# Kernel tuning notes

Hardware: AMD Instinct MI355X
Metric: run time of the kernel (lower is better)

## Reference

```python
import jax, jax.numpy as jnp
import numpy as np

TOPK = 13
NUM_CLASSES = 80
ALPHA = 1.0
BETA = 3.0
EPS = 1e-9
K_NEAR = 4
N_BINS = 36  # theta bins: arange(0, 360, 10)


def _dist_max_per_bin(anc_points, gt_pts):
    """gt_pts: (bs,nm,360,2), anc_points: (na,2) -> (bs,nm,na,36) ray targets."""
    d = gt_pts[:, :, None, :, :] - anc_points[None, None, :, None, :]  # (bs,nm,na,360,2)
    dist = jnp.sqrt(jnp.sum(d * d, axis=-1))                           # (bs,nm,na,360)
    ang = jnp.rad2deg(jnp.arctan2(d[..., 1], d[..., 0])) % 360.0       # (bs,nm,na,360)
    theta = jnp.arange(0, 360, 360 // N_BINS).astype(ang.dtype)        # (36,)

    def per_theta(th):
        diff = jnp.abs(ang - th)
        diff = jnp.where(diff > 180.0, 360.0 - diff, diff)
        neg_v, idx = jax.lax.top_k(-diff, K_NEAR)   # 4 nearest-angle contour pts
        val = -neg_v
        dk = jnp.take_along_axis(dist, idx, axis=-1)
        dk = jnp.where(jnp.min(val, axis=-1, keepdims=True) > 3.0, 1e-6, dk)
        return jnp.max(dk, axis=-1)                 # (bs,nm,na)

    dm = jax.lax.map(per_theta, theta)              # (36,bs,nm,na); chunked to bound memory
    return jnp.maximum(jnp.moveaxis(dm, 0, -1), 1e-6)


def _mask_iou(target, pred):
    l_max = jnp.maximum(target, pred)
    l_min = jnp.maximum(jnp.minimum(target, pred), 1e-6)
    return jnp.sum(l_min, -1) / jnp.sum(l_max, -1)


def _forward(pd_scores, pd_bboxes, anc_points, gt_labels, gt_bboxes, mask_gt, gt_coor):
    bs, na, nc = pd_scores.shape
    nm = gt_bboxes.shape[1]
    gl = gt_labels[..., 0]            # (bs,nm) int
    mgt = mask_gt[..., 0]             # (bs,nm) float
    gt_pts = gt_coor.reshape(bs, nm, 360, 2)

    # select_candidates_in_gts: anchor center strictly inside gt box
    lt, rb = gt_bboxes[..., :2], gt_bboxes[..., 2:]
    deltas = jnp.concatenate([anc_points[None, None] - lt[:, :, None],
                              rb[:, :, None] - anc_points[None, None]], axis=-1)
    mask_in_gts = (jnp.min(deltas, -1) > 1e-9).astype(pd_scores.dtype)  # (bs,nm,na)
    mask_sel = (mask_in_gts * mgt[:, :, None]) > 0

    # get_box_metrics_polar (dense over (bs,nm,na) instead of boolean-mask select)
    dist_max = _dist_max_per_bin(anc_points, gt_pts)                    # (bs,nm,na,36)
    overlaps = jnp.where(mask_sel, _mask_iou(dist_max, pd_bboxes[:, None]), 0.0)
    bbox_scores = jnp.take_along_axis(jnp.swapaxes(pd_scores, 1, 2), gl[:, :, None], axis=1)
    bbox_scores = jnp.where(mask_sel, bbox_scores, 0.0)
    align_metric = (bbox_scores ** ALPHA) * (overlaps ** BETA)

    # select_topk_candidates
    _, topk_idxs = jax.lax.top_k(align_metric, TOPK)
    topk_idxs = jnp.where(mgt[:, :, None] > 0, topk_idxs, 0)
    count = jnp.sum(jax.nn.one_hot(topk_idxs, na, dtype=align_metric.dtype), axis=-2)
    mask_topk = jnp.where(count > 1, 0.0, count)
    mask_pos = mask_topk * mask_in_gts * mgt[:, :, None]

    # select_highest_overlaps
    fg = jnp.sum(mask_pos, -2)                                          # (bs,na)
    multi = fg[:, None, :] > 1
    is_max = jnp.moveaxis(jax.nn.one_hot(jnp.argmax(overlaps, 1), nm, dtype=mask_pos.dtype), -1, 1)
    mask_pos = jnp.where(multi, is_max, mask_pos)
    fg_mask = jnp.sum(mask_pos, -2)
    target_gt_idx = jnp.argmax(mask_pos, -2)                            # (bs,na)

    # per-positive ray-distance targets + polar centerness (dense, masked)
    mask_pos_b = mask_pos > 0
    gt_dist = jnp.where(mask_pos_b[..., None], dist_max, 0.0)           # (bs,nm,na,36)
    cent = jnp.sqrt(jnp.min(dist_max, -1) / jnp.max(dist_max, -1))
    centerness_gt = jnp.where(mask_pos_b, cent, 0.0)                    # (bs,nm,na)

    # get_targets
    target_labels = jnp.maximum(jnp.take_along_axis(gl, target_gt_idx, axis=1), 0)
    target_bboxes = jnp.take_along_axis(gt_bboxes, target_gt_idx[..., None], axis=1)
    target_scores = jax.nn.one_hot(target_labels, NUM_CLASSES, dtype=pd_scores.dtype)
    target_scores = jnp.where((fg_mask > 0)[..., None], target_scores, 0.0)

    am = align_metric * mask_pos
    pos_align = jnp.max(am, -1, keepdims=True)
    pos_ov = jnp.max(overlaps * mask_pos, -1, keepdims=True)
    norm_align = jnp.max(am * pos_ov / (pos_align + EPS), -2)[..., None]  # (bs,na,1)
    target_scores = target_scores * norm_align

    return (target_labels, target_bboxes, target_scores, mask_pos_b,
            target_gt_idx, gt_dist, centerness_gt, fg_mask > 0)


def setup_inputs():
    key = jax.random.key(0)
    k = jax.random.split(key, 6)
    bs, nc, nm = 2, 80, 10
    pts, strs = [], []
    for s in (8, 16, 32):  # 640x640 YOLO grid -> 8400 anchors
        n = 640 // s
        yv, xv = np.meshgrid(np.arange(n), np.arange(n), indexing='ij')
        pts.append(np.stack([(xv + 0.5) * s, (yv + 0.5) * s], -1).reshape(-1, 2))
        strs.append(np.full((pts[-1].shape[0], 1), s, dtype=np.float32))
    anc_points = jnp.asarray(np.concatenate(pts).astype(np.float32))
    stride_tensor = jnp.asarray(np.concatenate(strs))
    na = anc_points.shape[0]
    pd_scores = jax.random.uniform(k[0], (bs, na, nc), dtype=jnp.float32)
    pd_bboxes = jax.random.uniform(k[1], (bs, na, 36), dtype=jnp.float32) * 100.0 + 1.0
    gt_labels = jax.random.randint(k[2], (bs, nm, 1), 0, nc)
    ctr = jax.random.uniform(k[3], (bs, nm, 2), dtype=jnp.float32) * 440.0 + 100.0
    wh = jax.random.uniform(k[4], (bs, nm, 2), dtype=jnp.float32) * 140.0 + 40.0
    gt_bboxes = jnp.concatenate([ctr - wh / 2.0, ctr + wh / 2.0], -1)
    th = jnp.arange(360.0) * (jnp.pi / 180.0)
    rad = (jnp.min(wh, -1, keepdims=True) / 2.0) * (0.6 + 0.4 * jax.random.uniform(k[5], (bs, nm, 360), dtype=jnp.float32))
    ray = jnp.stack([jnp.cos(th), jnp.sin(th)], -1)  # (360,2)
    gt_coor = (ctr[:, :, None, :] + rad[..., None] * ray[None, None]).reshape(bs, nm, 720)
    mask_gt = jnp.ones((bs, nm, 1), dtype=jnp.float32).at[1, 7:].set(0.0)
    return dict(pd_scores=pd_scores, pd_bboxes=pd_bboxes, anc_points=anc_points,
                gt_labels=gt_labels, gt_bboxes=gt_bboxes, mask_gt=mask_gt,
                gt_coor=gt_coor, stride_tensor=stride_tensor, ss=640,
                gt_center=ctr, imgsz=640)


def reference(pd_scores, pd_bboxes, anc_points, gt_labels, gt_bboxes, mask_gt, gt_coor, stride_tensor, ss, gt_center, imgsz):
    # ss, gt_center, imgsz, stride_tensor are accepted (as in the torch signature) but unused
    return _forward(pd_scores, pd_bboxes, anc_points, gt_labels, gt_bboxes, mask_gt, gt_coor)
```

## Files before the change

kernel.cpp:

```cpp
#include <hip/hip_runtime.h>

#define BS 2
#define NM 10
#define NA 8400
#define NC 80
#define NBIN 36
#define KTOP 13
#define NRECT (BS*NM*3)
#define WDIST_CAP 16384

typedef unsigned long long ull;

__device__ __forceinline__ void rect_one(int bm, int lv,
    const float* __restrict__ gtb, const float* __restrict__ mgt,
    int& x0, int& y0, int& cx, int& cy, int& cnt, int& n, int& base){
  cnt = 0; x0 = 0; y0 = 0; cx = 0; cy = 0; n = 0; base = 0;
  if (mgt[bm] > 0.f){
    float s = (float)(8 << lv);
    n = 640 >> (3 + lv);
    base = (lv == 0) ? 0 : ((lv == 1) ? 6400 : 8000);
    float lx = gtb[bm*4+0], ly = gtb[bm*4+1];
    float rx = gtb[bm*4+2], ry = gtb[bm*4+3];
    int a0 = (int)ceilf(lx/s - 0.5f); a0 = min(max(a0, 0), n);
    while (a0 > 0   &&  (((a0-1)+0.5f)*s - lx > 1e-9f)) a0--;
    while (a0 < n   && !(((a0  )+0.5f)*s - lx > 1e-9f)) a0++;
    int a1 = (int)floorf(rx/s - 0.5f); a1 = min(max(a1, -1), n-1);
    while (a1 < n-1 &&  (rx - ((a1+1)+0.5f)*s > 1e-9f)) a1++;
    while (a1 >= 0  && !(rx - ((a1  )+0.5f)*s > 1e-9f)) a1--;
    int b0 = (int)ceilf(ly/s - 0.5f); b0 = min(max(b0, 0), n);
    while (b0 > 0   &&  (((b0-1)+0.5f)*s - ly > 1e-9f)) b0--;
    while (b0 < n   && !(((b0  )+0.5f)*s - ly > 1e-9f)) b0++;
    int b1 = (int)floorf(ry/s - 0.5f); b1 = min(max(b1, -1), n-1);
    while (b1 < n-1 &&  (ry - ((b1+1)+0.5f)*s > 1e-9f)) b1++;
    while (b1 >= 0  && !(ry - ((b1  )+0.5f)*s > 1e-9f)) b1--;
    cx = max(0, a1 - a0 + 1);
    cy = max(0, b1 - b0 + 1);
    cnt = cx * cy;
    x0 = a0; y0 = b0;
  }
}

__device__ __forceinline__ void rect_setup(int tid,
    const float* __restrict__ gtb, const float* __restrict__ mgt,
    int* sx0, int* sy0, int* scx, int* scy, int* scum, int* sn, int* sbase){
  if (tid < NRECT){
    int bm = tid/3, lv = tid - bm*3;
    int x0, y0, cx, cy, cnt, n, base;
    rect_one(bm, lv, gtb, mgt, x0, y0, cx, cy, cnt, n, base);
    sx0[tid] = x0; sy0[tid] = y0; scx[tid] = cx; scy[tid] = cy;
    scum[tid] = cnt; sn[tid] = n; sbase[tid] = base;
  }
  __syncthreads();
  if (tid == 0){
    int acc = 0;
    for (int r = 0; r < NRECT; r++){ int c = scum[r]; scum[r] = acc; acc += c; }
    scum[NRECT] = acc;
  }
  __syncthreads();
}

__device__ __forceinline__ int pair_from_p(int p,
    const int* sx0, const int* sy0, const int* scx,
    const int* scum, const int* sn, const int* sbase){
  int lo = 0, hi = NRECT - 1;
  while (lo < hi){ int mid = (lo + hi + 1) >> 1; if (scum[mid] <= p) lo = mid; else hi = mid - 1; }
  int r = lo;
  int idx = p - scum[r];
  int cx = scx[r];
  int yi = idx / cx;
  int xi = idx - yi*cx;
  int a = sbase[r] + (sy0[r] + yi)*sn[r] + (sx0[r] + xi);
  int bm = r/3;
  return bm*NA + a;
}

__device__ __forceinline__ ull shflx_u64(ull v, int off){
  unsigned lo = (unsigned)v, hi = (unsigned)(v >> 32);
  lo = __shfl_xor(lo, off); hi = __shfl_xor(hi, off);
  return ((ull)hi << 32) | lo;
}

__global__ __launch_bounds__(256)
void k_dist(const float* __restrict__ pds, const float* __restrict__ pdb,
            const float* __restrict__ anc, const int* __restrict__ gl,
            const float* __restrict__ gtb, const float* __restrict__ mgt,
            const float* __restrict__ coor,
            float* __restrict__ out, float* __restrict__ wf){
  float* o_labels  = out;
  float* o_bboxes  = o_labels + BS*NA;
  float* o_scores  = o_bboxes + BS*NA*4;
  float* o_maskpos = o_scores + (size_t)BS*NA*NC;
  float* o_gtidx   = o_maskpos + BS*NM*NA;
  float* o_gtdist  = o_gtidx + BS*NA;
  float* o_cent    = o_gtdist + (size_t)BS*NM*NA*NBIN;
  float* o_fg      = o_cent + BS*NM*NA;

  float* w_align = wf + 16;
  float* w_ovl   = w_align + BS*NM*NA;
  float* w_dist  = w_ovl + BS*NM*NA;

  __shared__ int sx0[NRECT], sy0[NRECT], scx[NRECT], scy[NRECT], scum[NRECT+1], sn[NRECT], sbase[NRECT];
  __shared__ float2 s_ad[360];
  __shared__ unsigned short s_ix[360];
  __shared__ int s_cnt[NBIN], s_off[NBIN+1], s_cur[NBIN];
  __shared__ ull  s_k[NBIN*29];
  __shared__ float s_d[NBIN*29];
  __shared__ float s_res[NBIN];
  __shared__ int s_fbl[NBIN];
  __shared__ int s_nfb;

  float2* s_tmp = (float2*)s_k;
  unsigned char* s_bu = ((unsigned char*)s_k) + 2880;

  int tid = threadIdx.x;
  int lane = tid & 63, wave = tid >> 6;

  rect_setup(tid, gtb, mgt, sx0, sy0, scx, scy, scum, sn, sbase);
  int total = scum[NRECT];

  {
    int gtid = blockIdx.x*256 + tid, gsz = gridDim.x*256;
    float4 z4 = make_float4(0.f,0.f,0.f,0.f);
    float4* zs = (float4*)o_scores;
    for (int i = gtid; i < (BS*NA*NC)/4; i += gsz) zs[i] = z4;
    float4* zg = (float4*)o_gtdist;
    for (int i = gtid; i < (BS*NM*NA*NBIN)/4; i += gsz) zg[i] = z4;
    float4* zc = (float4*)o_cent;
    for (int i = gtid; i < (BS*NM*NA)/4; i += gsz) zc[i] = z4;
    float4* zm = (float4*)o_maskpos;
    for (int i = gtid; i < (BS*NM*NA)/4; i += gsz) zm[i] = z4;
    if (gtid < 16) wf[gtid] = 0.f;
    for (int t = gtid; t < BS*NA; t += gsz){
      int b = t / NA;
      o_gtidx[t] = 0.f;
      o_fg[t] = 0.f;
      int lbl = gl[b*NM]; if (lbl < 0) lbl = 0;
      o_labels[t] = (float)lbl;
      const float* bx = gtb + (b*NM)*4;
      ((float4*)o_bboxes)[t] = make_float4(bx[0], bx[1], bx[2], bx[3]);
    }
    for (int row = gtid; row < BS*NM*NA; row += gsz){
      int bm = row / NA;
      int a  = row - bm*NA;
      int lv = (a < 6400) ? 0 : ((a < 8000) ? 1 : 2);
      int ai = a - ((lv == 0) ? 0 : ((lv == 1) ? 6400 : 8000));
      int r = bm*3 + lv;
      bool inrect = false;
      if (scx[r] > 0 && scy[r] > 0){
        int n = sn[r];
        int y = ai / n, x = ai - y*n;
        inrect = (x >= sx0[r] && x < sx0[r]+scx[r] &&
                  y >= sy0[r] && y < sy0[r]+scy[r]);
      }
      if (!inrect) w_ovl[row] = 0.f;
    }
  }

  if (tid < NBIN) s_cnt[tid] = 0;
  if (tid == 0) s_nfb = 0;
  __syncthreads();

  int bin7 = tid % 36;
  int slot7 = tid / 36;

  for (int p = blockIdx.x; p < total; p += gridDim.x){
    int t = pair_from_p(p, sx0, sy0, scx, scum, sn, sbase);
    int a = t % NA; int bm = t / NA; int b = bm / NM;
    float ax = anc[2*a], ay = anc[2*a+1];
    const float* cc = coor + bm*720;

    for (int i = tid; i < 360; i += 256){
      float dx = cc[2*i]   - ax;
      float dy = cc[2*i+1] - ay;
      float dist = sqrtf(dx*dx + dy*dy);
      float an = atan2f(dy, dx) * 57.29577951308232f;
      if (an < 0.f) an += 360.f;
      int bu = (int)(an * 0.1f); bu = min(bu, NBIN-1);
      s_tmp[i] = make_float2(an, dist);
      s_bu[i] = (unsigned char)bu;
      atomicAdd(&s_cnt[bu], 1);
    }
    __syncthreads();
    if (wave == 0){
      int c = (lane < NBIN) ? s_cnt[lane] : 0;
      int incl = c;
#pragma unroll
      for (int st = 1; st < 64; st <<= 1){
        int o = __shfl_up(incl, st);
        if (lane >= st) incl += o;
      }
      if (lane < NBIN){ s_off[lane+1] = incl; s_cur[lane] = incl - c; }
      if (lane == 0) s_off[0] = 0;
    }
    __syncthreads();
    for (int i = tid; i < 360; i += 256){
      int bu = s_bu[i];
      float2 ad = s_tmp[i];
      int pos = atomicAdd(&s_cur[bu], 1);
      s_ad[pos] = ad;
      s_ix[pos] = (unsigned short)i;
    }
    __syncthreads();

#define EVALJ(J, TH) { \
      float2 ad = s_ad[J]; \
      unsigned int ixv = s_ix[J]; \
      float df = fabsf(ad.x - (TH)); \
      df = fminf(df, 360.f - df); \
      ull key = ((ull)__float_as_uint(df) << 32) | ixv; \
      if (key < k3){ \
        k3 = key; d3 = ad.y; \
        if (k3 < k2){ ull tk=k2; k2=k3; k3=tk; float td=d2; d2=d3; d3=td; } \
        if (k2 < k1){ ull tk=k1; k1=k2; k2=tk; float td=d1; d1=d2; d2=td; } \
        if (k1 < k0){ ull tk=k0; k0=k1; k1=tk; float td=d0; d0=d1; d1=td; } \
      } }

    if (slot7 < 7){
      float th = (float)(bin7*10);
      int r0s, r0e, r1s, r1e;
      if (bin7 == 0)      { r0s = s_off[35]; r0e = s_off[36]; r1s = 0; r1e = s_off[2]; }
      else if (bin7 == 35){ r0s = s_off[34]; r0e = s_off[36]; r1s = 0; r1e = s_off[1]; }
      else                { r0s = s_off[bin7-1]; r0e = s_off[bin7+2]; r1s = 0; r1e = 0; }
      int L0 = r0e - r0s, L = L0 + (r1e - r1s);
      ull k0,k1,k2,k3; float d0,d1,d2,d3;
      k0=k1=k2=k3=~0ull; d0=d1=d2=d3=0.f;
      for (int w = slot7; w < L; w += 7){
        int j = (w < L0) ? (r0s + w) : (r1s + w - L0);
        EVALJ(j, th)
      }
      int mb = bin7*29 + slot7*4;
      s_k[mb+0]=k0; s_k[mb+1]=k1; s_k[mb+2]=k2; s_k[mb+3]=k3;
      s_d[mb+0]=d0; s_d[mb+1]=d1; s_d[mb+2]=d2; s_d[mb+3]=d3;
    }
    __syncthreads();

    if (wave == 0 && lane < NBIN){
      int mb = lane*29;
      ull h0=s_k[mb+0], h1=s_k[mb+4],  h2=s_k[mb+8],  h3=s_k[mb+12],
          h4=s_k[mb+16], h5=s_k[mb+20], h6=s_k[mb+24];
      int p0=0,p1=0,p2=0,p3=0,p4=0,p5=0,p6=0;
      float v0m = 0.f, d4v = 0.f, dmax = 0.f;
#pragma unroll
      for (int step = 0; step < 4; step++){
        ull bk = h0; int bw = 0;
        if (h1 < bk){ bk = h1; bw = 1; }
        if (h2 < bk){ bk = h2; bw = 2; }
        if (h3 < bk){ bk = h3; bw = 3; }
        if (h4 < bk){ bk = h4; bw = 4; }
        if (h5 < bk){ bk = h5; bw = 5; }
        if (h6 < bk){ bk = h6; bw = 6; }
        float dd;
        if (bw == 0){ dd = s_d[mb   +p0]; p0++; h0 = (p0<4)? s_k[mb   +p0] : ~0ull; }
        else if (bw == 1){ dd = s_d[mb+ 4+p1]; p1++; h1 = (p1<4)? s_k[mb+ 4+p1] : ~0ull; }
        else if (bw == 2){ dd = s_d[mb+ 8+p2]; p2++; h2 = (p2<4)? s_k[mb+ 8+p2] : ~0ull; }
        else if (bw == 3){ dd = s_d[mb+12+p3]; p3++; h3 = (p3<4)? s_k[mb+12+p3] : ~0ull; }
        else if (bw == 4){ dd = s_d[mb+16+p4]; p4++; h4 = (p4<4)? s_k[mb+16+p4] : ~0ull; }
        else if (bw == 5){ dd = s_d[mb+20+p5]; p5++; h5 = (p5<4)? s_k[mb+20+p5] : ~0ull; }
        else             { dd = s_d[mb+24+p6]; p6++; h6 = (p6<4)? s_k[mb+24+p6] : ~0ull; }
        if (step == 0) v0m = __uint_as_float((unsigned)(bk >> 32));
        if (step == 3) d4v = __uint_as_float((unsigned)(bk >> 32));
        dmax = fmaxf(dmax, dd);
      }
      if (!(v0m <= 3.0f)){
        s_res[lane] = 1e-6f;
      } else if (!(d4v <= 9.99f)){
        int fi = atomicAdd(&s_nfb, 1);
        s_fbl[fi] = lane;
      } else {
        s_res[lane] = fmaxf(dmax, 1e-6f);
      }
    }
    __syncthreads();

    int nfb = s_nfb;
    if (nfb > 0){
      for (int f = wave; f < nfb; f += 4){
        int fb = s_fbl[f];
        float th = (float)(fb*10);
        ull k0,k1,k2,k3; float d0,d1,d2,d3;
        k0=k1=k2=k3=~0ull; d0=d1=d2=d3=0.f;
        for (int j = lane; j < 360; j += 64){
          EVALJ(j, th)
        }
        ull hk = k0; float hd = d0; int hp = 0;
        float dmax = 0.f;
#pragma unroll
        for (int r = 0; r < 4; r++){
          ull mk = hk; float md = hd;
#pragma unroll
          for (int off = 1; off < 64; off <<= 1){
            ull ok = shflx_u64(mk, off);
            float od = __shfl_xor(md, off);
            if (ok < mk){ mk = ok; md = od; }
          }
          if (hk == mk){
            hp++;
            hk = (hp==1)? k1 : (hp==2)? k2 : (hp==3)? k3 : ~0ull;
            hd = (hp==1)? d1 : (hp==2)? d2 : (hp==3)? d3 : 0.f;
          }
          dmax = fmaxf(dmax, md);
        }
        if (lane == 0) s_res[fb] = fmaxf(dmax, 1e-6f);
      }
    }
    __syncthreads();
#undef EVALJ

    if (wave == 0){
      float sum_min = 0.f, sum_max = 0.f;
      if (lane < NBIN){
        float dfin = s_res[lane];
        if (p < WDIST_CAP) w_dist[(size_t)p*NBIN + lane] = dfin;
        float pr = pdb[((size_t)b*NA + a)*NBIN + lane];
        sum_max = fmaxf(dfin, pr);
        sum_min = fmaxf(fminf(dfin, pr), 1e-6f);
      }
      for (int off = 32; off > 0; off >>= 1){
        sum_min += __shfl_down(sum_min, off);
        sum_max += __shfl_down(sum_max, off);
      }
      if (lane == 0){
        float ov = sum_min / sum_max;
        int cls = gl[bm];
        float sc = pds[((size_t)b*NA + a)*NC + cls];
        w_align[t] = sc * ov * ov * ov;
        w_ovl[t]   = ov;
      }
    }
    if (tid < NBIN) s_cnt[tid] = 0;
    if (tid == 0) s_nfb = 0;
    __syncthreads();
  }
}

__global__ __launch_bounds__(256)
void k_tail(const float* __restrict__ gtb, const float* __restrict__ mgt,
            const float* __restrict__ w_align, const float* __restrict__ w_ovl,
            const float* __restrict__ w_dist, const int* __restrict__ gl,
            float* __restrict__ o_labels, float* __restrict__ o_bboxes,
            float* __restrict__ o_maskpos, float* __restrict__ o_gtidx,
            float* __restrict__ o_fg,
            float* __restrict__ o_gtdist, float* __restrict__ o_cent,
            float* __restrict__ o_scores,
            int* __restrict__ w_sel, int* __restrict__ done){
  __shared__ int sx0[NRECT], sy0[NRECT], scx[NRECT], scy[NRECT], scum[NRECT+1], sn[NRECT], sbase[NRECT];
  __shared__ float sv[256*KTOP];
  __shared__ int   si[256*KTOP];
  __shared__ float wv4[4];
  __shared__ int   wi4[4];
  __shared__ int   sel[BS*NM*KTOP];
  __shared__ unsigned paB[BS*NM], poB[BS*NM];
  __shared__ int fcnt;
  __shared__ int   fT[BS*NM*KTOP];
  __shared__ int   fA[BS*NM*KTOP];
  __shared__ int   fL[BS*NM*KTOP];
  __shared__ float fV[BS*NM*KTOP];
  __shared__ int sLast;

  int tid = threadIdx.x;
  int lane = tid & 63, wave = tid >> 6;

  rect_setup(tid, gtb, mgt, sx0, sy0, scx, scy, scum, sn, sbase);

  int bm = blockIdx.x;
  {
    const float* al = w_align + (size_t)bm*NA;
    int pbase = scum[bm*3], pm1 = scum[bm*3+1], pm2 = scum[bm*3+2], pend = scum[bm*3+3];

    float v[KTOP]; int ix[KTOP];
#pragma unroll
    for (int j = 0; j < KTOP; j++){ v[j] = -1.f; ix[j] = 0x7fffffff; }
    for (int p = pbase + tid; p < pend; p += 256){
      int r = bm*3 + ((p >= pm1) + (p >= pm2));
      int idx = p - scum[r];
      int cx = scx[r];
      int yi = idx / cx;
      int xi = idx - yi*cx;
      int a = sbase[r] + (sy0[r] + yi)*sn[r] + (sx0[r] + xi);
      float x = al[a];
      if (x > v[KTOP-1]){
        v[KTOP-1] = x; ix[KTOP-1] = a;
#pragma unroll
        for (int j = KTOP-1; j > 0; j--){
          if (v[j] > v[j-1]){
            float tv = v[j-1]; v[j-1] = v[j]; v[j] = tv;
            int   ti = ix[j-1]; ix[j-1] = ix[j]; ix[j] = ti;
          }
        }
      }
    }
#pragma unroll
    for (int j = 0; j < KTOP; j++){ sv[tid*KTOP+j] = v[j]; si[tid*KTOP+j] = ix[j]; }

    int head = 0;
    for (int r = 0; r < KTOP; r++){
      float cv = sv[tid*KTOP + head];
      int   ci = si[tid*KTOP + head];
      float rv = cv; int ri = ci;
      for (int off = 32; off > 0; off >>= 1){
        float ov = __shfl_down(rv, off);
        int   oi = __shfl_down(ri, off);
        if (ov > rv || (ov == rv && oi < ri)){ rv = ov; ri = oi; }
      }
      if (lane == 0){ wv4[wave] = rv; wi4[wave] = ri; }
      __syncthreads();
      float Wv = wv4[0]; int Wi = wi4[0];
#pragma unroll
      for (int w = 1; w < 4; w++){
        float ov = wv4[w]; int oi = wi4[w];
        if (ov > Wv || (ov == Wv && oi < Wi)){ Wv = ov; Wi = oi; }
      }
      if (ci == Wi && head < KTOP-1) head++;
      if (tid == 0)
        __hip_atomic_store(&w_sel[bm*KTOP + r], (Wv > 0.f) ? Wi : -1,
                           __ATOMIC_RELAXED, __HIP_MEMORY_SCOPE_AGENT);
      __syncthreads();
    }
  }

  if (tid == 0){
    __threadfence();
    int old = __hip_atomic_fetch_add(done, 1, __ATOMIC_ACQ_REL, __HIP_MEMORY_SCOPE_AGENT);
    sLast = (old == BS*NM - 1) ? 1 : 0;
  }
  __syncthreads();
  if (!sLast) return;

  for (int s = tid; s < BS*NM*KTOP; s += 256)
    sel[s] = __hip_atomic_load(&w_sel[s], __ATOMIC_RELAXED, __HIP_MEMORY_SCOPE_AGENT);
  if (tid < BS*NM){ paB[tid] = 0u; poB[tid] = 0u; }
  if (tid == 0) fcnt = 0;
  __syncthreads();

  for (int s = tid; s < BS*NM*KTOP; s += 256){
    int a = sel[s];
    if (a >= 0){
      int sbm = s / KTOP;
      int b   = sbm / NM;
      int s0 = b*NM*KTOP;
      int cnt = 0, minS = 1 << 30;
      for (int s2 = s0; s2 < s0 + NM*KTOP; s2++){
        if (sel[s2] == a){ cnt++; if (s2 < minS) minS = s2; }
      }
      if (s == minS){
        int bi = sbm - b*NM;
        if (cnt > 1){
          float bv = -1.f; bi = 0;
#pragma unroll
          for (int mm = 0; mm < NM; mm++){
            float vv = w_ovl[((size_t)(b*NM+mm))*NA + a];
            if (vv > bv){ bv = vv; bi = mm; }
          }
        }
        int bmw = b*NM + bi;
        int ta  = b*NA + a;
        o_maskpos[(size_t)bmw*NA + a] = 1.f;
        o_gtidx[ta] = (float)bi;
        o_fg[ta] = 1.f;
        int lbl = gl[bmw]; if (lbl < 0) lbl = 0;
        o_labels[ta] = (float)lbl;
        const float* bx = gtb + bmw*4;
        ((float4*)o_bboxes)[ta] = make_float4(bx[0], bx[1], bx[2], bx[3]);
        float av  = w_align[(size_t)bmw*NA + a];
        float ovv = w_ovl[(size_t)bmw*NA + a];
        atomicMax(&paB[bmw], __float_as_uint(av));
        atomicMax(&poB[bmw], __float_as_uint(ovv));
        int j = atomicAdd(&fcnt, 1);
        fT[j] = bmw*NA + a; fA[j] = ta; fL[j] = lbl; fV[j] = av;
      }
    }
  }
  __syncthreads();

  int nf = fcnt;
  for (int j = tid; j < nf; j += 256){
    int tf = fT[j];
    int a = tf % NA; int bmw = tf / NA;
    int lv = (a < 6400) ? 0 : ((a < 8000) ? 1 : 2);
    int ai = a - ((lv == 0) ? 0 : ((lv == 1) ? 6400 : 8000));
    int r = bmw*3 + lv;
    int n = sn[r];
    int y = ai / n, x = ai - y*n;
    int p = scum[r] + (y - sy0[r])*scx[r] + (x - sx0[r]);
    const float4* src = (const float4*)(w_dist + (size_t)p*NBIN);
    float4* dst = (float4*)(o_gtdist + (size_t)tf*NBIN);
    float vmin = 1e30f, vmax = 0.f;
#pragma unroll
    for (int q = 0; q < 9; q++){
      float4 v4 = src[q];
      dst[q] = v4;
      vmin = fminf(vmin, fminf(fminf(v4.x, v4.y), fminf(v4.z, v4.w)));
      vmax = fmaxf(vmax, fmaxf(fmaxf(v4.x, v4.y), fmaxf(v4.z, v4.w)));
    }
    o_cent[tf] = sqrtf(vmin / vmax);
    float paf = __uint_as_float(paB[bmw]);
    float pof = __uint_as_float(poB[bmw]);
    o_scores[(size_t)fA[j]*NC + fL[j]] = fV[j] * pof / (paf + 1e-9f);
  }
}

extern "C" void kernel_launch(void* const* d_in, const int* in_sizes, int n_in,
                              void* d_out, int out_size, void* d_ws, size_t ws_size,
                              hipStream_t stream){
  const float* pds  = (const float*)d_in[0];
  const float* pdb  = (const float*)d_in[1];
  const float* anc  = (const float*)d_in[2];
  const int*   gl   = (const int*)  d_in[3];
  const float* gtb  = (const float*)d_in[4];
  const float* mgt  = (const float*)d_in[5];
  const float* coor = (const float*)d_in[6];

  float* out = (float*)d_out;
  float* o_labels  = out;
  float* o_bboxes  = o_labels + BS*NA;
  float* o_scores  = o_bboxes + BS*NA*4;
  float* o_maskpos = o_scores + (size_t)BS*NA*NC;
  float* o_gtidx   = o_maskpos + BS*NM*NA;
  float* o_gtdist  = o_gtidx + BS*NA;
  float* o_cent    = o_gtdist + (size_t)BS*NM*NA*NBIN;
  float* o_fg      = o_cent + BS*NM*NA;

  float* wf      = (float*)d_ws;
  int*   done    = (int*)d_ws;
  float* w_align = wf + 16;
  float* w_ovl   = w_align + BS*NM*NA;
  float* w_dist  = w_ovl + BS*NM*NA;
  int*   w_sel   = (int*)(w_dist + (size_t)WDIST_CAP*NBIN);

  k_dist<<<4096, 256, 0, stream>>>(pds, pdb, anc, gl, gtb, mgt, coor, out, wf);
  k_tail<<<BS*NM, 256, 0, stream>>>(gtb, mgt, w_align, w_ovl, w_dist, gl,
                                    o_labels, o_bboxes, o_maskpos, o_gtidx, o_fg,
                                    o_gtdist, o_cent, o_scores, w_sel, done);
}
```

Baseline: 158.1 us.

## Restructure per-pair top-4 selection with quad shuffles and fewer barriers

Each of the 36 bins now gets 4 adjacent lanes that scan candidates and merge their partial top-4 lists with xor shuffles, replacing the 7-slot shared-memory merge and one block barrier. The contour points stay in registers instead of a shared staging buffer. Counters are reset earlier, the fallback barrier runs only when fallback bins exist, and the score and box loads are hoisted to the loop start. The rect prefix scan uses a wave shuffle scan, and the grid is halved, so each block processes more pairs.

```diff
diff --git a/kernel.cpp b/kernel.cpp
--- a/kernel.cpp
+++ b/kernel.cpp
@@ -51,10 +51,16 @@
     scum[tid] = cnt; sn[tid] = n; sbase[tid] = base;
   }
   __syncthreads();
-  if (tid == 0){
-    int acc = 0;
-    for (int r = 0; r < NRECT; r++){ int c = scum[r]; scum[r] = acc; acc += c; }
-    scum[NRECT] = acc;
+  if (tid < 64){
+    int c = (tid < NRECT) ? scum[tid] : 0;
+    int incl = c;
+#pragma unroll
+    for (int st = 1; st < 64; st <<= 1){
+      int o = __shfl_up(incl, st);
+      if (tid >= st) incl += o;
+    }
+    if (tid < NRECT) scum[tid] = incl - c;
+    if (tid == NRECT-1) scum[NRECT] = incl;
   }
   __syncthreads();
 }
@@ -103,14 +109,9 @@
   __shared__ float2 s_ad[360];
   __shared__ unsigned short s_ix[360];
   __shared__ int s_cnt[NBIN], s_off[NBIN+1], s_cur[NBIN];
-  __shared__ ull  s_k[NBIN*29];
-  __shared__ float s_d[NBIN*29];
   __shared__ float s_res[NBIN];
   __shared__ int s_fbl[NBIN];
   __shared__ int s_nfb;
-
-  float2* s_tmp = (float2*)s_k;
-  unsigned char* s_bu = ((unsigned char*)s_k) + 2880;
 
   int tid = threadIdx.x;
   int lane = tid & 63, wave = tid >> 6;
@@ -160,8 +161,8 @@
   if (tid == 0) s_nfb = 0;
   __syncthreads();
 
-  int bin7 = tid % 36;
-  int slot7 = tid / 36;
+  int bin4 = tid >> 2;
+  int slot4 = tid & 3;
 
   for (int p = blockIdx.x; p < total; p += gridDim.x){
     int t = pair_from_p(p, sx0, sy0, scx, scum, sn, sbase);
@@ -169,18 +170,36 @@
     float ax = anc[2*a], ay = anc[2*a+1];
     const float* cc = coor + bm*720;
 
-    for (int i = tid; i < 360; i += 256){
+    float pr = 0.f, sc = 0.f;
+    if (wave == 0){
+      if (lane < NBIN) pr = pdb[((size_t)b*NA + a)*NBIN + lane];
+      int cls = gl[bm];
+      sc = pds[((size_t)b*NA + a)*NC + cls];
+    }
+
+    float an0, di0, an1 = 0.f, di1 = 0.f;
+    int bu0, bu1 = -1;
+    {
+      float dx = cc[2*tid]   - ax;
+      float dy = cc[2*tid+1] - ay;
+      di0 = sqrtf(dx*dx + dy*dy);
+      an0 = atan2f(dy, dx) * 57.29577951308232f;
+      if (an0 < 0.f) an0 += 360.f;
+      bu0 = min((int)(an0 * 0.1f), NBIN-1);
+      atomicAdd(&s_cnt[bu0], 1);
+    }
+    if (tid < 104){
+      int i = tid + 256;
       float dx = cc[2*i]   - ax;
       float dy = cc[2*i+1] - ay;
-      float dist = sqrtf(dx*dx + dy*dy);
-      float an = atan2f(dy, dx) * 57.29577951308232f;
-      if (an < 0.f) an += 360.f;
-      int bu = (int)(an * 0.1f); bu = min(bu, NBIN-1);
-      s_tmp[i] = make_float2(an, dist);
-      s_bu[i] = (unsigned char)bu;
-      atomicAdd(&s_cnt[bu], 1);
+      di1 = sqrtf(dx*dx + dy*dy);
+      an1 = atan2f(dy, dx) * 57.29577951308232f;
+      if (an1 < 0.f) an1 += 360.f;
+      bu1 = min((int)(an1 * 0.1f), NBIN-1);
+      atomicAdd(&s_cnt[bu1], 1);
     }
     __syncthreads();
+
     if (wave == 0){
       int c = (lane < NBIN) ? s_cnt[lane] : 0;
       int incl = c;
@@ -193,12 +212,18 @@
       if (lane == 0) s_off[0] = 0;
     }
     __syncthreads();
-    for (int i = tid; i < 360; i += 256){
-      int bu = s_bu[i];
-      float2 ad = s_tmp[i];
-      int pos = atomicAdd(&s_cur[bu], 1);
-      s_ad[pos] = ad;
-      s_ix[pos] = (unsigned short)i;
+
+    if (tid < NBIN) s_cnt[tid] = 0;
+    if (tid == 64) s_nfb = 0;
+    {
+      int pos = atomicAdd(&s_cur[bu0], 1);
+      s_ad[pos] = make_float2(an0, di0);
+      s_ix[pos] = (unsigned short)tid;
+    }
+    if (bu1 >= 0){
+      int pos = atomicAdd(&s_cur[bu1], 1);
+      s_ad[pos] = make_float2(an1, di1);
+      s_ix[pos] = (unsigned short)(tid + 256);
     }
     __syncthreads();
 
@@ -215,59 +240,41 @@
         if (k1 < k0){ ull tk=k0; k0=k1; k1=tk; float td=d0; d0=d1; d1=td; } \
       } }
 
-    if (slot7 < 7){
-      float th = (float)(bin7*10);
+    if (bin4 < NBIN){
+      float th = (float)(bin4*10);
       int r0s, r0e, r1s, r1e;
-      if (bin7 == 0)      { r0s = s_off[35]; r0e = s_off[36]; r1s = 0; r1e = s_off[2]; }
-      else if (bin7 == 35){ r0s = s_off[34]; r0e = s_off[36]; r1s = 0; r1e = s_off[1]; }
-      else                { r0s = s_off[bin7-1]; r0e = s_off[bin7+2]; r1s = 0; r1e = 0; }
+      if (bin4 == 0)      { r0s = s_off[35]; r0e = s_off[36]; r1s = 0; r1e = s_off[2]; }
+      else if (bin4 == 35){ r0s = s_off[34]; r0e = s_off[36]; r1s = 0; r1e = s_off[1]; }
+      else                { r0s = s_off[bin4-1]; r0e = s_off[bin4+2]; r1s = 0; r1e = 0; }
       int L0 = r0e - r0s, L = L0 + (r1e - r1s);
       ull k0,k1,k2,k3; float d0,d1,d2,d3;
       k0=k1=k2=k3=~0ull; d0=d1=d2=d3=0.f;
-      for (int w = slot7; w < L; w += 7){
+      for (int w = slot4; w < L; w += 4){
         int j = (w < L0) ? (r0s + w) : (r1s + w - L0);
         EVALJ(j, th)
       }
-      int mb = bin7*29 + slot7*4;
-      s_k[mb+0]=k0; s_k[mb+1]=k1; s_k[mb+2]=k2; s_k[mb+3]=k3;
-      s_d[mb+0]=d0; s_d[mb+1]=d1; s_d[mb+2]=d2; s_d[mb+3]=d3;
-    }
-    __syncthreads();
-
-    if (wave == 0 && lane < NBIN){
-      int mb = lane*29;
-      ull h0=s_k[mb+0], h1=s_k[mb+4],  h2=s_k[mb+8],  h3=s_k[mb+12],
-          h4=s_k[mb+16], h5=s_k[mb+20], h6=s_k[mb+24];
-      int p0=0,p1=0,p2=0,p3=0,p4=0,p5=0,p6=0;
       float v0m = 0.f, d4v = 0.f, dmax = 0.f;
 #pragma unroll
-      for (int step = 0; step < 4; step++){
-        ull bk = h0; int bw = 0;
-        if (h1 < bk){ bk = h1; bw = 1; }
-        if (h2 < bk){ bk = h2; bw = 2; }
-        if (h3 < bk){ bk = h3; bw = 3; }
-        if (h4 < bk){ bk = h4; bw = 4; }
-        if (h5 < bk){ bk = h5; bw = 5; }
-        if (h6 < bk){ bk = h6; bw = 6; }
-        float dd;
-        if (bw == 0){ dd = s_d[mb   +p0]; p0++; h0 = (p0<4)? s_k[mb   +p0] : ~0ull; }
-        else if (bw == 1){ dd = s_d[mb+ 4+p1]; p1++; h1 = (p1<4)? s_k[mb+ 4+p1] : ~0ull; }
-        else if (bw == 2){ dd = s_d[mb+ 8+p2]; p2++; h2 = (p2<4)? s_k[mb+ 8+p2] : ~0ull; }
-        else if (bw == 3){ dd = s_d[mb+12+p3]; p3++; h3 = (p3<4)? s_k[mb+12+p3] : ~0ull; }
-        else if (bw == 4){ dd = s_d[mb+16+p4]; p4++; h4 = (p4<4)? s_k[mb+16+p4] : ~0ull; }
-        else if (bw == 5){ dd = s_d[mb+20+p5]; p5++; h5 = (p5<4)? s_k[mb+20+p5] : ~0ull; }
-        else             { dd = s_d[mb+24+p6]; p6++; h6 = (p6<4)? s_k[mb+24+p6] : ~0ull; }
-        if (step == 0) v0m = __uint_as_float((unsigned)(bk >> 32));
-        if (step == 3) d4v = __uint_as_float((unsigned)(bk >> 32));
-        dmax = fmaxf(dmax, dd);
-      }
-      if (!(v0m <= 3.0f)){
-        s_res[lane] = 1e-6f;
-      } else if (!(d4v <= 9.99f)){
-        int fi = atomicAdd(&s_nfb, 1);
-        s_fbl[fi] = lane;
-      } else {
-        s_res[lane] = fmaxf(dmax, 1e-6f);
+      for (int r = 0; r < 4; r++){
+        ull mk = k0; float md = d0;
+        ull ok = shflx_u64(mk, 1); float od = __shfl_xor(md, 1);
+        if (ok < mk){ mk = ok; md = od; }
+        ok = shflx_u64(mk, 2); od = __shfl_xor(md, 2);
+        if (ok < mk){ mk = ok; md = od; }
+        if (r == 0) v0m = __uint_as_float((unsigned)(mk >> 32));
+        if (r == 3) d4v = __uint_as_float((unsigned)(mk >> 32));
+        dmax = fmaxf(dmax, md);
+        if (k0 == mk){ k0=k1; d0=d1; k1=k2; d1=d2; k2=k3; d2=d3; k3=~0ull; d3=0.f; }
+      }
+      if (slot4 == 0){
+        if (!(v0m <= 3.0f)){
+          s_res[bin4] = 1e-6f;
+        } else if (!(d4v <= 9.99f)){
+          int fi = atomicAdd(&s_nfb, 1);
+          s_fbl[fi] = bin4;
+        } else {
+          s_res[bin4] = fmaxf(dmax, 1e-6f);
+        }
       }
     }
     __syncthreads();
@@ -302,8 +309,8 @@
         }
         if (lane == 0) s_res[fb] = fmaxf(dmax, 1e-6f);
       }
-    }
-    __syncthreads();
+      __syncthreads();
+    }
 #undef EVALJ
 
     if (wave == 0){
@@ -311,7 +318,6 @@
       if (lane < NBIN){
         float dfin = s_res[lane];
         if (p < WDIST_CAP) w_dist[(size_t)p*NBIN + lane] = dfin;
-        float pr = pdb[((size_t)b*NA + a)*NBIN + lane];
         sum_max = fmaxf(dfin, pr);
         sum_min = fmaxf(fminf(dfin, pr), 1e-6f);
       }
@@ -321,14 +327,10 @@
       }
       if (lane == 0){
         float ov = sum_min / sum_max;
-        int cls = gl[bm];
-        float sc = pds[((size_t)b*NA + a)*NC + cls];
         w_align[t] = sc * ov * ov * ov;
         w_ovl[t]   = ov;
       }
     }
-    if (tid < NBIN) s_cnt[tid] = 0;
-    if (tid == 0) s_nfb = 0;
     __syncthreads();
   }
 }
@@ -527,7 +529,7 @@
   float* w_dist  = w_ovl + BS*NM*NA;
   int*   w_sel   = (int*)(w_dist + (size_t)WDIST_CAP*NBIN);
 
-  k_dist<<<4096, 256, 0, stream>>>(pds, pdb, anc, gl, gtb, mgt, coor, out, wf);
+  k_dist<<<2048, 256, 0, stream>>>(pds, pdb, anc, gl, gtb, mgt, coor, out, wf);
   k_tail<<<BS*NM, 256, 0, stream>>>(gtb, mgt, w_align, w_ovl, w_dist, gl,
                                     o_labels, o_bboxes, o_maskpos, o_gtidx, o_fg,
                                     o_gtdist, o_cent, o_scores, w_sel, done);
```

Measured after the change: 154.7 us. 1.02x faster.
